# Kernel optimization log

Hardware: AMD Instinct MI355X
Metric: run time of the kernel (lower is better)

## Reference

```python
import jax, jax.numpy as jnp
import numpy as np

B, L, N, DOUT = 8, 8192, 256, 256  # batch, seq_len, state_dim, output_dim


def setup_inputs() -> dict:
    key = jax.random.key(0)
    k_u, k_h, k_w = jax.random.split(key, 3)
    u = jax.random.normal(k_u, (B, L, 1), dtype=jnp.float32)
    # impulse response buffer (stands in for A_bar^i @ B_bar rows); decay-scaled for realism
    h = jax.random.normal(k_h, (L, N), dtype=jnp.float32) * 0.02
    W = jax.random.normal(k_w, (DOUT, N), dtype=jnp.float32) * (1.0 / np.sqrt(N))
    return {"u": u, "h": h, "W": W}


def reference(u, h, W):
    L_ = h.shape[0]
    n_fft = 2 * L_
    # FFT-based long convolution: U:[B, n_fft//2+1, 1], H:[n_fft//2+1, N]
    U = jnp.fft.rfft(u, n=n_fft, axis=1)
    H = jnp.fft.rfft(h, n=n_fft, axis=0)
    M = U * H[None, :, :]                      # broadcast channel 1 -> N
    m = jnp.fft.irfft(M, n=n_fft, axis=1)[:, :L_, :]  # [B, L, N]
    return jnp.einsum('bln,on->blo', m, W)     # Linear(state_dim -> output_dim), no bias
```

## Files before the change

### kernel.cpp

```cpp
#include <hip/hip_runtime.h>
#include <hip/hip_bf16.h>
#include <stdint.h>
#include <stddef.h>

typedef __attribute__((ext_vector_type(4))) float f32x4;
typedef __attribute__((ext_vector_type(8))) short s16x8;

#define B_    8
#define L_    8192
#define N_    256
#define DOUT_ 256

__device__ __forceinline__ unsigned short f2bf(float f) {
  unsigned int x = __float_as_uint(f);
  x += 0x7fff + ((x >> 16) & 1);
  return (unsigned short)(x >> 16);
}

__global__ void k_zero(float* __restrict__ out) {
  int t = blockIdx.x * 256 + threadIdx.x;
  int b = t >> 18;
  int r = t & 262143;
  f32x4 z = {0.f, 0.f, 0.f, 0.f};
  *(f32x4*)(out + (size_t)b * 2097152 + 1048576 + (size_t)r * 4) = z;
}

__global__ void k_urev(const float* __restrict__ u, unsigned short* __restrict__ urev) {
  int t = blockIdx.x * 256 + threadIdx.x;
  int b = t >> 14;
  int j = t & 16383;
  unsigned short v = 0;
  if (j <= 8191) v = f2bf(u[b * L_ + 8191 - j]);
  urev[t] = v;
}

__global__ void k_amat(const unsigned short* __restrict__ urev, unsigned short* __restrict__ Am) {
  int t = blockIdx.x * 256 + threadIdx.x;
  int i0 = (t & 15) * 8;
  int lp = (t >> 4) & 127;
  int r2 = t >> 11;
  int d  = r2 % 65;
  int b  = r2 / 65;
  s16x8 v;
#pragma unroll
  for (int j = 0; j < 8; ++j) v[j] = 0;
  if (d < 64) {
    const unsigned short* ur = urev + b * 16384;
    int jbase = 8191 - 128 * d - lp + i0;
#pragma unroll
    for (int j = 0; j < 8; ++j) v[j] = (short)ur[jbase + j];
  }
  *(s16x8*)(Am + (size_t)t * 8) = v;
}

__global__ void k_gt(const float* __restrict__ W, const float* __restrict__ h,
                     unsigned short* __restrict__ gT) {
  int gid  = blockIdx.x * 256 + threadIdx.x;
  int lane = gid & 63;
  int wid  = gid >> 6;
  int o_t  = wid >> 7;
  int i_t  = wid & 127;
  int o0 = o_t * 16, i0 = i_t * 64;
  int ln = lane & 15, hi = lane >> 4;
  f32x4 acc[4] = {};
#pragma unroll
  for (int k0 = 0; k0 < N_; k0 += 32) {
    const float* wp = W + (o0 + ln) * N_ + k0 + 8 * hi;
    float4 w0 = *(const float4*)wp;
    float4 w1 = *(const float4*)(wp + 4);
    s16x8 a;
    a[0] = (short)f2bf(w0.x); a[1] = (short)f2bf(w0.y);
    a[2] = (short)f2bf(w0.z); a[3] = (short)f2bf(w0.w);
    a[4] = (short)f2bf(w1.x); a[5] = (short)f2bf(w1.y);
    a[6] = (short)f2bf(w1.z); a[7] = (short)f2bf(w1.w);
#pragma unroll
    for (int ns = 0; ns < 4; ++ns) {
      const float* hp = h + (size_t)(i0 + 16 * ns + ln) * N_ + k0 + 8 * hi;
      float4 h0 = *(const float4*)hp;
      float4 h1 = *(const float4*)(hp + 4);
      s16x8 bb;
      bb[0] = (short)f2bf(h0.x); bb[1] = (short)f2bf(h0.y);
      bb[2] = (short)f2bf(h0.z); bb[3] = (short)f2bf(h0.w);
      bb[4] = (short)f2bf(h1.x); bb[5] = (short)f2bf(h1.y);
      bb[6] = (short)f2bf(h1.z); bb[7] = (short)f2bf(h1.w);
      acc[ns] = __builtin_amdgcn_mfma_f32_16x16x32_bf16(a, bb, acc[ns], 0, 0, 0);
    }
  }
#pragma unroll
  for (int ns = 0; ns < 4; ++ns)
#pragma unroll
    for (int q = 0; q < 4; ++q)
      gT[(size_t)(o0 + 4 * hi + q) * L_ + i0 + 16 * ns + ln] = f2bf(acc[ns][q]);
}

__global__ __launch_bounds__(512, 2) void k_main(const unsigned short* __restrict__ Am,
                                                 const unsigned short* __restrict__ gT,
                                                 float* __restrict__ out) {
  __shared__ short As[2][16384];
  __shared__ short Bs[2][16384];
  const int half = blockIdx.x;
  const int b    = blockIdx.y;
  const int zp   = blockIdx.z;
  const int Rb = 31 - zp, Rs = zp;
  const int nktb = 4 * (Rb + 1);
  const int s_lo = half ? 66 : 0;
  const int s_hi = half ? 132 : 66;
  const int tid = threadIdx.x;
  const int lane = tid & 63;
  const int w = tid >> 6;
  const int wr = w >> 2, wc = w & 3;
  const int ln = lane & 15, hi = lane >> 4;

  const int t3 = tid >> 3;
  const int sA = ((tid & 7) ^ (t3 & 7)) << 3;
  const unsigned short* AmB = Am + (size_t)(b * 65) * 16384;
  const unsigned short* Bq[4] = {
    gT + (size_t)(t3)       * L_ + sA,
    gT + (size_t)(t3 + 64)  * L_ + sA,
    gT + (size_t)(t3 + 128) * L_ + sA,
    gT + (size_t)(t3 + 192) * L_ + sA };
  const int rl0 = t3, rl1 = 64 + t3;

  const int offA = (wr * 128 + ln) * 64;
  const int offB = (wc * 64 + ln) * 64;
  const int sw = ln & 7;
  const int k0o = (hi ^ sw) * 8;
  const int k1o = ((hi + 4) ^ sw) * 8;

  float* outb = out + (size_t)b * (L_ * DOUT_);
  f32x4 acc[8][4] = {};

#define ISSUE_A(Rv, ktv, dst, q) do { \
    int dd = 2 * (Rv) + ((q) >> 1) - ((ktv) >> 1); \
    int sd = dd < 0 ? 64 : dd; \
    const unsigned short* src = AmB + ((size_t)sd << 14) + (((q) & 1 ? rl1 : rl0) << 7) + (((ktv) & 1) << 6) + sA; \
    __builtin_amdgcn_global_load_lds((const __attribute__((address_space(1))) void*)src, \
        (__attribute__((address_space(3))) void*)((dst) + (tid + 512 * (q)) * 8), 16, 0, 0); \
  } while (0)

#define ISSUE_B(ktv, dst, q) do { \
    const unsigned short* src = Bq[q] + (ktv) * 64; \
    __builtin_amdgcn_global_load_lds((const __attribute__((address_space(1))) void*)src, \
        (__attribute__((address_space(3))) void*)((dst) + (tid + 512 * (q)) * 8), 16, 0, 0); \
  } while (0)

  auto flush = [&](int R, bool atomic) {
    const int l0 = R * 256 + wr * 128 + 4 * hi;
    const int o0 = wc * 64 + ln;
#pragma unroll
    for (int m = 0; m < 8; ++m)
#pragma unroll
      for (int q = 0; q < 4; ++q) {
        float* rowp = outb + (size_t)(l0 + m * 16 + q) * DOUT_ + o0;
#pragma unroll
        for (int n = 0; n < 4; ++n) {
          if (atomic) atomicAdd(rowp + n * 16, acc[m][n][q]);
          else        rowp[n * 16] = acc[m][n][q];
        }
      }
#pragma unroll
    for (int m = 0; m < 8; ++m)
#pragma unroll
      for (int n = 0; n < 4; ++n)
        acc[m][n] = (f32x4){0.f, 0.f, 0.f, 0.f};
  };

  {
    short* Aw = &As[s_lo & 1][0];
    short* Bw = &Bs[s_lo & 1][0];
    const int kt0 = s_lo;
    ISSUE_A(Rb, kt0, Aw, 0); ISSUE_A(Rb, kt0, Aw, 1);
    ISSUE_A(Rb, kt0, Aw, 2); ISSUE_A(Rb, kt0, Aw, 3);
    ISSUE_B(kt0, Bw, 0); ISSUE_B(kt0, Bw, 1);
    ISSUE_B(kt0, Bw, 2); ISSUE_B(kt0, Bw, 3);
  }

  for (int s = s_lo; s < s_hi; ++s) {
    asm volatile("s_waitcnt vmcnt(0)" ::: "memory");
    __builtin_amdgcn_sched_barrier(0);
    __builtin_amdgcn_s_barrier();
    __builtin_amdgcn_sched_barrier(0);

    if (half && s == nktb) flush(Rb, true);

    const short* Ac = &As[s & 1][0];
    const short* Bc = &Bs[s & 1][0];
    short* Aw = &As[(s + 1) & 1][0];
    short* Bw = &Bs[(s + 1) & 1][0];
    const int s1  = (s + 1 < s_hi) ? s + 1 : s;
    const int R1  = (s1 < nktb) ? Rb : Rs;
    const int kt1 = (s1 < nktb) ? s1 : s1 - nktb;

    s16x8 bf[4], af[4];
#pragma unroll
    for (int n = 0; n < 4; ++n) bf[n] = *(const s16x8*)(Bc + offB + n * 1024 + k0o);
    ISSUE_A(R1, kt1, Aw, 0); ISSUE_A(R1, kt1, Aw, 1);
#pragma unroll
    for (int m = 0; m < 4; ++m) af[m] = *(const s16x8*)(Ac + offA + m * 1024 + k0o);
    __builtin_amdgcn_s_setprio(1);
#pragma unroll
    for (int m = 0; m < 4; ++m)
#pragma unroll
      for (int n = 0; n < 4; ++n)
        acc[m][n] = __builtin_amdgcn_mfma_f32_16x16x32_bf16(af[m], bf[n], acc[m][n], 0, 0, 0);
    __builtin_amdgcn_s_setprio(0);
    ISSUE_A(R1, kt1, Aw, 2); ISSUE_A(R1, kt1, Aw, 3);
#pragma unroll
    for (int m = 0; m < 4; ++m) af[m] = *(const s16x8*)(Ac + offA + 4096 + m * 1024 + k0o);
    __builtin_amdgcn_s_setprio(1);
#pragma unroll
    for (int m = 0; m < 4; ++m)
#pragma unroll
      for (int n = 0; n < 4; ++n)
        acc[4 + m][n] = __builtin_amdgcn_mfma_f32_16x16x32_bf16(af[m], bf[n], acc[4 + m][n], 0, 0, 0);
    __builtin_amdgcn_s_setprio(0);
#pragma unroll
    for (int n = 0; n < 4; ++n) bf[n] = *(const s16x8*)(Bc + offB + n * 1024 + k1o);
    ISSUE_B(kt1, Bw, 0); ISSUE_B(kt1, Bw, 1);
#pragma unroll
    for (int m = 0; m < 4; ++m) af[m] = *(const s16x8*)(Ac + offA + m * 1024 + k1o);
    __builtin_amdgcn_s_setprio(1);
#pragma unroll
    for (int m = 0; m < 4; ++m)
#pragma unroll
      for (int n = 0; n < 4; ++n)
        acc[m][n] = __builtin_amdgcn_mfma_f32_16x16x32_bf16(af[m], bf[n], acc[m][n], 0, 0, 0);
    __builtin_amdgcn_s_setprio(0);
    ISSUE_B(kt1, Bw, 2); ISSUE_B(kt1, Bw, 3);
#pragma unroll
    for (int m = 0; m < 4; ++m) af[m] = *(const s16x8*)(Ac + offA + 4096 + m * 1024 + k1o);
    __builtin_amdgcn_s_setprio(1);
#pragma unroll
    for (int m = 0; m < 4; ++m)
#pragma unroll
      for (int n = 0; n < 4; ++n)
        acc[4 + m][n] = __builtin_amdgcn_mfma_f32_16x16x32_bf16(af[m], bf[n], acc[4 + m][n], 0, 0, 0);
    __builtin_amdgcn_s_setprio(0);
  }

  asm volatile("s_waitcnt vmcnt(0)" ::: "memory");

  if (half) flush(Rs, false);
  else      flush(Rb, true);

#undef ISSUE_A
#undef ISSUE_B
}

extern "C" void kernel_launch(void* const* d_in, const int* in_sizes, int n_in,
                              void* d_out, int out_size, void* d_ws, size_t ws_size,
                              hipStream_t stream) {
  const float* u = (const float*)d_in[0];
  const float* h = (const float*)d_in[1];
  const float* W = (const float*)d_in[2];
  float* out = (float*)d_out;

  char* ws = (char*)d_ws;
  const size_t AM_BYTES = (size_t)8 * 65 * 16384 * 2;
  unsigned short* Am   = (unsigned short*)ws;
  unsigned short* gT   = (unsigned short*)(ws + AM_BYTES);
  unsigned short* urev = (unsigned short*)(ws + AM_BYTES + (size_t)4 * 1024 * 1024);

  k_zero<<<8192, 256, 0, stream>>>(out);
  k_urev<<<512, 256, 0, stream>>>(u, urev);
  k_amat<<<4160, 256, 0, stream>>>(urev, Am);
  k_gt<<<512, 256, 0, stream>>>(W, h, gT);
  k_main<<<dim3(2, 8, 16), 512, 0, stream>>>(Am, gT, out);
}
```

Before: 188.2 us.

## Restructure GEMM main loop into four-phase quadrant schedule with partial vmcnt waits

```diff
diff --git a/kernel.cpp b/kernel.cpp
--- a/kernel.cpp
+++ b/kernel.cpp
@@ -121,8 +121,8 @@
     gT + (size_t)(t3 + 192) * L_ + sA };
   const int rl0 = t3, rl1 = 64 + t3;
 
-  const int offA = (wr * 128 + ln) * 64;
-  const int offB = (wc * 64 + ln) * 64;
+  const int baseA0 = (wr * 64 + ln) * 64;
+  const int baseB0 = (wc * 32 + ln) * 64;
   const int sw = ln & 7;
   const int k0o = (hi ^ sw) * 8;
   const int k1o = ((hi + 4) ^ sw) * 8;
@@ -145,19 +145,20 @@
   } while (0)
 
   auto flush = [&](int R, bool atomic) {
-    const int l0 = R * 256 + wr * 128 + 4 * hi;
-    const int o0 = wc * 64 + ln;
-#pragma unroll
-    for (int m = 0; m < 8; ++m)
+#pragma unroll
+    for (int m = 0; m < 8; ++m) {
+      const int mrow = (m < 4) ? wr * 64 + m * 16 : 128 + wr * 64 + (m - 4) * 16;
 #pragma unroll
       for (int q = 0; q < 4; ++q) {
-        float* rowp = outb + (size_t)(l0 + m * 16 + q) * DOUT_ + o0;
+        float* rowp = outb + (size_t)(R * 256 + mrow + 4 * hi + q) * DOUT_;
 #pragma unroll
         for (int n = 0; n < 4; ++n) {
-          if (atomic) atomicAdd(rowp + n * 16, acc[m][n][q]);
-          else        rowp[n * 16] = acc[m][n][q];
+          const int ncol = ((n < 2) ? wc * 32 + n * 16 : 128 + wc * 32 + (n - 2) * 16) + ln;
+          if (atomic) atomicAdd(rowp + ncol, acc[m][n][q]);
+          else        rowp[ncol] = acc[m][n][q];
         }
       }
+    }
 #pragma unroll
     for (int m = 0; m < 8; ++m)
 #pragma unroll
@@ -168,74 +169,110 @@
   {
     short* Aw = &As[s_lo & 1][0];
     short* Bw = &Bs[s_lo & 1][0];
-    const int kt0 = s_lo;
-    ISSUE_A(Rb, kt0, Aw, 0); ISSUE_A(Rb, kt0, Aw, 1);
-    ISSUE_A(Rb, kt0, Aw, 2); ISSUE_A(Rb, kt0, Aw, 3);
-    ISSUE_B(kt0, Bw, 0); ISSUE_B(kt0, Bw, 1);
-    ISSUE_B(kt0, Bw, 2); ISSUE_B(kt0, Bw, 3);
+    ISSUE_A(Rb, s_lo, Aw, 0); ISSUE_A(Rb, s_lo, Aw, 1);
+    ISSUE_B(s_lo, Bw, 0); ISSUE_B(s_lo, Bw, 1);
+    ISSUE_B(s_lo, Bw, 2); ISSUE_B(s_lo, Bw, 3);
+    ISSUE_A(Rb, s_lo, Aw, 2); ISSUE_A(Rb, s_lo, Aw, 3);
+    asm volatile("s_waitcnt vmcnt(0)" ::: "memory");
+    __builtin_amdgcn_s_barrier();
   }
 
   for (int s = s_lo; s < s_hi; ++s) {
-    asm volatile("s_waitcnt vmcnt(0)" ::: "memory");
-    __builtin_amdgcn_sched_barrier(0);
-    __builtin_amdgcn_s_barrier();
-    __builtin_amdgcn_sched_barrier(0);
-
     if (half && s == nktb) flush(Rb, true);
 
-    const short* Ac = &As[s & 1][0];
-    const short* Bc = &Bs[s & 1][0];
-    short* Aw = &As[(s + 1) & 1][0];
-    short* Bw = &Bs[(s + 1) & 1][0];
+    const int cur = s & 1;
+    const short* Ac = &As[cur][0];
+    const short* Bc = &Bs[cur][0];
+    short* Aw = &As[cur ^ 1][0];
+    short* Bw = &Bs[cur ^ 1][0];
     const int s1  = (s + 1 < s_hi) ? s + 1 : s;
     const int R1  = (s1 < nktb) ? Rb : Rs;
     const int kt1 = (s1 < nktb) ? s1 : s1 - nktb;
 
-    s16x8 bf[4], af[4];
-#pragma unroll
-    for (int n = 0; n < 4; ++n) bf[n] = *(const s16x8*)(Bc + offB + n * 1024 + k0o);
+    s16x8 af[4][2], bf[2][2], bg[2][2];
+
     ISSUE_A(R1, kt1, Aw, 0); ISSUE_A(R1, kt1, Aw, 1);
-#pragma unroll
-    for (int m = 0; m < 4; ++m) af[m] = *(const s16x8*)(Ac + offA + m * 1024 + k0o);
+    asm volatile("s_waitcnt vmcnt(4)" ::: "memory");
+#pragma unroll
+    for (int m = 0; m < 4; ++m) {
+      af[m][0] = *(const s16x8*)(Ac + baseA0 + m * 1024 + k0o);
+      af[m][1] = *(const s16x8*)(Ac + baseA0 + m * 1024 + k1o);
+    }
+#pragma unroll
+    for (int n = 0; n < 2; ++n) {
+      bf[n][0] = *(const s16x8*)(Bc + baseB0 + n * 1024 + k0o);
+      bf[n][1] = *(const s16x8*)(Bc + baseB0 + n * 1024 + k1o);
+    }
+    __builtin_amdgcn_s_barrier();
+    asm volatile("s_waitcnt lgkmcnt(0)" ::: "memory");
+    __builtin_amdgcn_sched_barrier(0);
     __builtin_amdgcn_s_setprio(1);
 #pragma unroll
-    for (int m = 0; m < 4; ++m)
-#pragma unroll
-      for (int n = 0; n < 4; ++n)
-        acc[m][n] = __builtin_amdgcn_mfma_f32_16x16x32_bf16(af[m], bf[n], acc[m][n], 0, 0, 0);
+    for (int kk = 0; kk < 2; ++kk)
+#pragma unroll
+      for (int m = 0; m < 4; ++m)
+#pragma unroll
+        for (int n = 0; n < 2; ++n)
+          acc[m][n] = __builtin_amdgcn_mfma_f32_16x16x32_bf16(af[m][kk], bf[n][kk], acc[m][n], 0, 0, 0);
     __builtin_amdgcn_s_setprio(0);
+    __builtin_amdgcn_s_barrier();
+
+    ISSUE_B(kt1, Bw, 0); ISSUE_B(kt1, Bw, 1);
+    asm volatile("s_waitcnt vmcnt(4)" ::: "memory");
+#pragma unroll
+    for (int n = 0; n < 2; ++n) {
+      bg[n][0] = *(const s16x8*)(Bc + baseB0 + 8192 + n * 1024 + k0o);
+      bg[n][1] = *(const s16x8*)(Bc + baseB0 + 8192 + n * 1024 + k1o);
+    }
+    __builtin_amdgcn_s_barrier();
+    asm volatile("s_waitcnt lgkmcnt(0)" ::: "memory");
+    __builtin_amdgcn_sched_barrier(0);
+    __builtin_amdgcn_s_setprio(1);
+#pragma unroll
+    for (int kk = 0; kk < 2; ++kk)
+#pragma unroll
+      for (int m = 0; m < 4; ++m)
+#pragma unroll
+        for (int n = 0; n < 2; ++n)
+          acc[m][n + 2] = __builtin_amdgcn_mfma_f32_16x16x32_bf16(af[m][kk], bg[n][kk], acc[m][n + 2], 0, 0, 0);
+    __builtin_amdgcn_s_setprio(0);
+    __builtin_amdgcn_s_barrier();
+
+    ISSUE_B(kt1, Bw, 2); ISSUE_B(kt1, Bw, 3);
+    asm volatile("s_waitcnt vmcnt(4)" ::: "memory");
+#pragma unroll
+    for (int m = 0; m < 4; ++m) {
+      af[m][0] = *(const s16x8*)(Ac + baseA0 + 8192 + m * 1024 + k0o);
+      af[m][1] = *(const s16x8*)(Ac + baseA0 + 8192 + m * 1024 + k1o);
+    }
+    __builtin_amdgcn_s_barrier();
+    asm volatile("s_waitcnt lgkmcnt(0)" ::: "memory");
+    __builtin_amdgcn_sched_barrier(0);
+    __builtin_amdgcn_s_setprio(1);
+#pragma unroll
+    for (int kk = 0; kk < 2; ++kk)
+#pragma unroll
+      for (int m = 0; m < 4; ++m)
+#pragma unroll
+        for (int n = 0; n < 2; ++n)
+          acc[4 + m][n] = __builtin_amdgcn_mfma_f32_16x16x32_bf16(af[m][kk], bf[n][kk], acc[4 + m][n], 0, 0, 0);
+    __builtin_amdgcn_s_setprio(0);
+    __builtin_amdgcn_s_barrier();
+
     ISSUE_A(R1, kt1, Aw, 2); ISSUE_A(R1, kt1, Aw, 3);
-#pragma unroll
-    for (int m = 0; m < 4; ++m) af[m] = *(const s16x8*)(Ac + offA + 4096 + m * 1024 + k0o);
+    asm volatile("s_waitcnt vmcnt(4)" ::: "memory");
+    __builtin_amdgcn_s_barrier();
+    __builtin_amdgcn_sched_barrier(0);
     __builtin_amdgcn_s_setprio(1);
 #pragma unroll
-    for (int m = 0; m < 4; ++m)
-#pragma unroll
-      for (int n = 0; n < 4; ++n)
-        acc[4 + m][n] = __builtin_amdgcn_mfma_f32_16x16x32_bf16(af[m], bf[n], acc[4 + m][n], 0, 0, 0);
+    for (int kk = 0; kk < 2; ++kk)
+#pragma unroll
+      for (int m = 0; m < 4; ++m)
+#pragma unroll
+        for (int n = 0; n < 2; ++n)
+          acc[4 + m][n + 2] = __builtin_amdgcn_mfma_f32_16x16x32_bf16(af[m][kk], bg[n][kk], acc[4 + m][n + 2], 0, 0, 0);
     __builtin_amdgcn_s_setprio(0);
-#pragma unroll
-    for (int n = 0; n < 4; ++n) bf[n] = *(const s16x8*)(Bc + offB + n * 1024 + k1o);
-    ISSUE_B(kt1, Bw, 0); ISSUE_B(kt1, Bw, 1);
-#pragma unroll
-    for (int m = 0; m < 4; ++m) af[m] = *(const s16x8*)(Ac + offA + m * 1024 + k1o);
-    __builtin_amdgcn_s_setprio(1);
-#pragma unroll
-    for (int m = 0; m < 4; ++m)
-#pragma unroll
-      for (int n = 0; n < 4; ++n)
-        acc[m][n] = __builtin_amdgcn_mfma_f32_16x16x32_bf16(af[m], bf[n], acc[m][n], 0, 0, 0);
-    __builtin_amdgcn_s_setprio(0);
-    ISSUE_B(kt1, Bw, 2); ISSUE_B(kt1, Bw, 3);
-#pragma unroll
-    for (int m = 0; m < 4; ++m) af[m] = *(const s16x8*)(Ac + offA + 4096 + m * 1024 + k1o);
-    __builtin_amdgcn_s_setprio(1);
-#pragma unroll
-    for (int m = 0; m < 4; ++m)
-#pragma unroll
-      for (int n = 0; n < 4; ++n)
-        acc[4 + m][n] = __builtin_amdgcn_mfma_f32_16x16x32_bf16(af[m], bf[n], acc[4 + m][n], 0, 0, 0);
-    __builtin_amdgcn_s_setprio(0);
+    __builtin_amdgcn_s_barrier();
   }
 
   asm volatile("s_waitcnt vmcnt(0)" ::: "memory");
```

New measurement: 265.1 us. 1.41x slower.
